# Optimization experiments

Hardware: AMD Instinct MI355X
Metric: run time of the kernel (lower is better)

The kernel has to match this reference:

```python
import jax, jax.numpy as jnp
import numpy as np

MAX_STEP = 4
G_HID = 16      # hidden_graph_num
S_HID = 10      # hidden_graph_size
D = 128         # embed_dim / hidden_dim
N = 100000      # total nodes across batch of session graphs
E = 640000      # total edges
B = 2048        # number of graphs (fixed num_segments)
VOCAB = 100000  # POI vocabulary
NEG_SLOPE = 0.01  # LeakyReLU default


def leaky(x):
    return jnp.where(x >= 0, x, NEG_SLOPE * x)


def setup_inputs() -> dict:
    key = jax.random.key(0)
    ks = jax.random.split(key, 10)
    x_idx = jax.random.randint(ks[0], (N,), 0, VOCAB)
    edge_index = jax.random.randint(ks[1], (2, E), 0, N)
    batch = jnp.sort(jax.random.randint(ks[2], (N,), 0, B))
    poi_emb = jax.random.normal(ks[3], (VOCAB, D), jnp.float32) * 0.02
    fc_w = jax.random.normal(ks[4], (D, D), jnp.float32) / np.sqrt(D)
    fc_b = jnp.zeros((D,), jnp.float32)
    hidden_adj = jax.random.normal(ks[5], (G_HID, S_HID * (S_HID - 1) // 2), jnp.float32)
    hidden_feat = jax.random.normal(ks[6], (G_HID, S_HID, D), jnp.float32)
    mlp_w = jax.random.normal(ks[7], (G_HID * MAX_STEP, D), jnp.float32) / np.sqrt(G_HID * MAX_STEP)
    mlp_b = jnp.zeros((D,), jnp.float32)
    return dict(x_idx=x_idx, edge_index=edge_index, batch=batch,
                poi_emb=poi_emb, fc_w=fc_w, fc_b=fc_b,
                hidden_adj=hidden_adj, hidden_feat=hidden_feat,
                mlp_w=mlp_w, mlp_b=mlp_b)


def reference(x_idx, edge_index, batch, poi_emb, fc_w, fc_b,
              hidden_adj, hidden_feat, mlp_w, mlp_b):
    # Symmetric hidden-graph adjacency from upper-triangular params
    iu, ju = np.triu_indices(S_HID, 1)
    A = jnp.zeros((G_HID, S_HID, S_HID), hidden_adj.dtype).at[:, iu, ju].set(leaky(hidden_adj))
    A = A + jnp.swapaxes(A, 1, 2)

    # Node features: embedding lookup -> Linear -> sigmoid  [N, D]
    x = jax.nn.sigmoid(poi_emb[x_idx] @ fc_w + fc_b)
    z = hidden_feat                                   # [G, S, D]
    zx = jnp.einsum('gsd,nd->gsn', z, x)              # [G, S, N]

    src, dst = edge_index[0], edge_index[1]
    outs = []
    for i in range(MAX_STEP):
        if i == 0:
            # eye @ z == z, so t == zx (faithful to the torch einsum chain)
            t = zx
        else:
            # MessagePassing.propagate with default add aggregation:
            # x_new[v] = sum_{(u->v) in E} x[u]
            x = jax.ops.segment_sum(x[src], dst, num_segments=N)
            z = jnp.einsum('gst,gtd->gsd', A, z)
            t = jnp.einsum('gsd,nd->gsn', z, x)
        t = zx * t                                    # dropout = identity (eval)
        # graph-wise scatter pooling: index_add over node axis -> [B, G, S]
        pooled = jax.ops.segment_sum(jnp.moveaxis(t, 2, 0), batch, num_segments=B)
        outs.append(pooled.sum(axis=2))               # [B, G]

    out = jnp.concatenate(outs, axis=1)               # [B, G*MAX_STEP]
    return leaky(out @ mlp_w + mlp_b)                 # [B, D]
```

## Files before the change

### kernel.cpp

```cpp
#include <hip/hip_runtime.h>
#include <hip/hip_bf16.h>
#include <math.h>

#define G_HID 16
#define S_HID 10
#define D 128
#define MAX_STEP 4
#define NEG 0.01f
#define SCAN_TILE 1024

typedef __attribute__((ext_vector_type(8))) short short8;
typedef __attribute__((ext_vector_type(4))) float f32x4;

__device__ __forceinline__ float leaky_f(float v){ return v >= 0.f ? v : NEG*v; }
__device__ __forceinline__ unsigned short f2bf(float f){
    unsigned int u = __float_as_uint(f);
    u = (u + 0x7FFFu + ((u>>16)&1u)) >> 16;
    return (unsigned short)u;
}
__device__ __forceinline__ float bf_lo(unsigned int v){ return __uint_as_float(v << 16); }
__device__ __forceinline__ float bf_hi(unsigned int v){ return __uint_as_float(v & 0xFFFF0000u); }

__global__ void prep_kernel(const float* __restrict__ hidden_adj,
                            const float* __restrict__ hidden_feat,
                            short* __restrict__ zpack)
{
    int g = blockIdx.x;
    __shared__ float Ag[S_HID][S_HID];
    __shared__ float zb[2][S_HID][D];
    int t = threadIdx.x;
    if (t < S_HID*S_HID) {
        int i = t / S_HID, j = t % S_HID;
        float v = 0.f;
        if (i < j) {
            int idx = 9*i - i*(i-1)/2 + (j - i - 1);
            v = leaky_f(hidden_adj[g*45 + idx]);
        } else if (i > j) {
            int idx = 9*j - j*(j-1)/2 + (i - j - 1);
            v = leaky_f(hidden_adj[g*45 + idx]);
        }
        Ag[i][j] = v;
    }
    for (int idx = t; idx < S_HID*D; idx += 128) {
        int s = idx / D, d = idx % D;
        zb[0][s][d] = hidden_feat[(g*S_HID + s)*D + d];
    }
    __syncthreads();
    int cur = 0;
    for (int step = 0; step < MAX_STEP; ++step) {
        if (step > 0) {
            int nxt = cur ^ 1;
            for (int idx = t; idx < S_HID*D; idx += 128) {
                int s = idx / D, d = idx % D;
                float acc = 0.f;
                #pragma unroll
                for (int u = 0; u < S_HID; ++u) acc += Ag[s][u] * zb[cur][u][d];
                zb[nxt][s][d] = acc;
            }
            cur = nxt;
            __syncthreads();
        }
        for (int idx = t; idx < S_HID*D; idx += 128) {
            int s = idx / D, k = idx % D;
            int row = g*S_HID + s;
            int tt = row >> 4, li = row & 15;
            int kt = k >> 5, q = (k >> 3) & 3, j = k & 7;
            zpack[(((step*10 + tt)*4 + kt)*64 + q*16 + li)*8 + j] = (short)f2bf(zb[cur][s][k]);
        }
        __syncthreads();
    }
}

__global__ void wpack_kernel(const float* __restrict__ fc_w, short* __restrict__ wp){
    int idx = blockIdx.x*256 + threadIdx.x;
    if (idx >= 16384) return;
    int j = idx & 7, lane = (idx >> 3) & 63, ctkt = idx >> 9;
    int ct = ctkt & 7, kt = ctkt >> 3;
    int k   = kt*32 + (lane >> 4)*8 + j;
    int col = ct*16 + (lane & 15);
    wp[idx] = (short)f2bf(fc_w[k*D + col]);
}

__global__ void count_kernel(const int* __restrict__ dst, int* __restrict__ offsets, int E){
    int e = blockIdx.x*blockDim.x + threadIdx.x;
    if (e < E) atomicAdd(&offsets[dst[e]+1], 1);
}

__global__ void scan1_kernel(int* __restrict__ data, int* __restrict__ bsums, int n){
    __shared__ int wsum[4];
    int base = blockIdx.x * SCAN_TILE + threadIdx.x*4;
    int v[4];
    #pragma unroll
    for (int j=0;j<4;++j) v[j] = (base+j < n) ? data[base+j] : 0;
    v[1]+=v[0]; v[2]+=v[1]; v[3]+=v[2];
    int lane = threadIdx.x & 63;
    int w = threadIdx.x >> 6;
    int s = v[3];
    for (int d=1; d<64; d<<=1){
        int o = __shfl_up(s, d);
        if (lane >= d) s += o;
    }
    if (lane == 63) wsum[w] = s;
    int sexc = s - v[3];
    __syncthreads();
    int woff = 0;
    for (int ww=0; ww<w; ++ww) woff += wsum[ww];
    int off = woff + sexc;
    #pragma unroll
    for (int j=0;j<4;++j) { if (base+j < n) data[base+j] = v[j] + off; }
    if (threadIdx.x == 255) bsums[blockIdx.x] = off + v[3];
}

__global__ void scan2_kernel(int* __restrict__ bsums, int nb){
    __shared__ int ws[4];
    __shared__ int carry_s;
    if (threadIdx.x == 0) carry_s = 0;
    __syncthreads();
    for (int start = 0; start < nb; start += 256){
        int i = start + (int)threadIdx.x;
        int v = (i < nb) ? bsums[i] : 0;
        int lane = threadIdx.x & 63, w = threadIdx.x >> 6;
        int s = v;
        for (int d=1; d<64; d<<=1){ int o = __shfl_up(s, d); if (lane >= d) s += o; }
        if (lane == 63) ws[w] = s;
        __syncthreads();
        int woff = 0;
        for (int ww=0; ww<w; ++ww) woff += ws[ww];
        int inc = s + woff + carry_s;
        if (i < nb) bsums[i] = inc - v;
        __syncthreads();
        if (threadIdx.x == 255) carry_s = inc;
        __syncthreads();
    }
}

__global__ void scan3_kernel(int* __restrict__ data, const int* __restrict__ bsums, int n){
    int base = blockIdx.x * SCAN_TILE + threadIdx.x*4;
    int add = bsums[blockIdx.x];
    #pragma unroll
    for (int j=0;j<4;++j){ if (base+j < n) data[base+j] += add; }
}

__global__ void fill_kernel(const int* __restrict__ src, const int* __restrict__ dst,
                            int* __restrict__ cursor, int* __restrict__ csr, int E){
    int e = blockIdx.x*blockDim.x + threadIdx.x;
    if (e < E){
        int d = dst[e];
        int pos = atomicAdd(&cursor[d], 1);
        csr[pos] = src[e];
    }
}


__device__ __forceinline__ void compute_slots(const int* __restrict__ batch, int n0, int N,
                                              int* slots, int* slotb, int* nslots_s, int t){
    if (t < 64) {
        int gn = n0 + t;
        int b = (gn < N) ? batch[gn] : -1;
        int bprev = -1;
        if (t > 0) bprev = (gn-1 < N) ? batch[gn-1] : -1;
        int flag = (t == 0 || b != bprev) ? 1 : 0;
        int s = flag;
        for (int d=1; d<64; d<<=1){ int o = __shfl_up(s, d); if (t >= d) s += o; }
        int slot = s - 1;
        slots[t] = slot;
        if (flag) slotb[slot] = b;
        if (t == 63) *nslots_s = s;
    }
}

template<int STEP0>
__device__ __forceinline__ void step_phase(const short8 bw[4],
                                 const short* __restrict__ zstep,
                                 float* Pf, float (*accs)[G_HID],
                                 const int* slots, const int* slotb, int nslots,
                                 uint2* __restrict__ y0buf, float* __restrict__ pooled,
                                 int stepoff, int t, int bid)
{
    int l = t & 63, w = t >> 6, li = l & 15, q = l >> 4;
    f32x4 accA[10];
    #pragma unroll
    for (int t10 = 0; t10 < 10; ++t10){
        f32x4 acc = (f32x4){0.f,0.f,0.f,0.f};
        #pragma unroll
        for (int kt = 0; kt < 4; ++kt){
            short8 az = *reinterpret_cast<const short8*>(&zstep[((t10*4 + kt)*64 + l)*8]);
            acc = __builtin_amdgcn_mfma_f32_16x16x32_bf16(az, bw[kt], acc, 0, 0, 0);
        }
        accA[t10] = acc;
    }
    size_t ybase = ((size_t)bid*4 + w)*10*64 + l;
    #pragma unroll
    for (int t10 = 0; t10 < 10; ++t10){
        f32x4 acc = accA[t10];
        float p0, p1, p2, p3;
        if (STEP0){
            uint2 st;
            st.x = (unsigned int)f2bf(acc[0]) | ((unsigned int)f2bf(acc[1]) << 16);
            st.y = (unsigned int)f2bf(acc[2]) | ((unsigned int)f2bf(acc[3]) << 16);
            y0buf[ybase + (size_t)t10*64] = st;
            p0 = acc[0]*acc[0]; p1 = acc[1]*acc[1]; p2 = acc[2]*acc[2]; p3 = acc[3]*acc[3];
        } else {
            uint2 v = y0buf[ybase + (size_t)t10*64];
            p0 = acc[0]*bf_lo(v.x); p1 = acc[1]*bf_hi(v.x);
            p2 = acc[2]*bf_lo(v.y); p3 = acc[3]*bf_hi(v.y);
        }
        int rb = (t10*16 + q*4)*66 + w*16 + li;
        Pf[rb]       = p0;
        Pf[rb + 66]  = p1;
        Pf[rb + 132] = p2;
        Pf[rb + 198] = p3;
    }
    __syncthreads();
    #pragma unroll
    for (int i = 0; i < 4; ++i){
        int g = t & 15, nd = (t >> 4) + i*16;
        float c = 0.f;
        #pragma unroll
        for (int s = 0; s < S_HID; ++s) c += Pf[(g*10 + s)*66 + nd];
        atomicAdd(&accs[slots[nd]][g], c);
    }
    __syncthreads();
    for (int idx = t; idx < nslots*G_HID; idx += 256){
        int j = idx >> 4, g = idx & 15;
        int b = slotb[j];
        if (b >= 0) atomicAdd(&pooled[(size_t)b*64 + stepoff + g], accs[j][g]);
    }
}

__global__ __launch_bounds__(256) void embed_step0_kernel(
        const int* __restrict__ x_idx, const float* __restrict__ poi_emb,
        const short* __restrict__ wp, const float* __restrict__ fc_b,
        const short* __restrict__ zstep, const int* __restrict__ batch,
        unsigned short* __restrict__ x0, uint2* __restrict__ y0buf,
        float* __restrict__ pooled, int N)
{
    __shared__ __align__(16) char lbuf[42240];
    __shared__ float accs[64][G_HID];
    __shared__ int slots[64];
    __shared__ int slotb[64];
    __shared__ int nslots_s;
    unsigned short* xs = (unsigned short*)lbuf;
    float* Pf = (float*)lbuf;
    int n0 = blockIdx.x * 64;
    int t = threadIdx.x;

    #pragma unroll
    for (int i = 0; i < 8; ++i) {
        int idx = t + i*256;
        int row = idx >> 5, c4 = (idx & 31)*4;
        int gn = n0 + row;
        float4 v = make_float4(0.f,0.f,0.f,0.f);
        if (gn < N) v = *reinterpret_cast<const float4*>(&poi_emb[(size_t)x_idx[gn]*D + c4]);
        unsigned int p0 = (unsigned int)f2bf(v.x) | ((unsigned int)f2bf(v.y) << 16);
        unsigned int p1 = (unsigned int)f2bf(v.z) | ((unsigned int)f2bf(v.w) << 16);
        *reinterpret_cast<uint2*>(&xs[row*136 + c4]) = make_uint2(p0, p1);
    }
    #pragma unroll
    for (int i = 0; i < 4; ++i) ((float*)accs)[t + i*256] = 0.f;
    compute_slots(batch, n0, N, slots, slotb, &nslots_s, t);
    __syncthreads();

    int l = t & 63, w = t >> 6, li = l & 15, q = l >> 4;
    short8 a[4];
    #pragma unroll
    for (int kt = 0; kt < 4; ++kt)
        a[kt] = *reinterpret_cast<const short8*>(&xs[(w*16 + li)*136 + kt*32 + q*8]);
    f32x4 facc[8];
    #pragma unroll
    for (int ct = 0; ct < 8; ++ct) facc[ct] = (f32x4){0.f,0.f,0.f,0.f};
    #pragma unroll
    for (int kt = 0; kt < 4; ++kt){
        #pragma unroll
        for (int ct = 0; ct < 8; ++ct){
            short8 b = reinterpret_cast<const short8*>(wp)[(kt*8 + ct)*64 + l];
            facc[ct] = __builtin_amdgcn_mfma_f32_16x16x32_bf16(a[kt], b, facc[ct], 0, 0, 0);
        }
    }
    #pragma unroll
    for (int ct = 0; ct < 8; ++ct){
        float bias = fc_b[ct*16 + li];
        #pragma unroll
        for (int r = 0; r < 4; ++r){
            int row = w*16 + q*4 + r;
            float s = (n0 + row < N) ? 1.f/(1.f + __expf(-(facc[ct][r] + bias))) : 0.f;
            xs[row*136 + ct*16 + li] = f2bf(s);
        }
    }
    __syncthreads();
    {
        int row = t >> 2, ch = t & 3, gn = n0 + row;
        if (gn < N){
            #pragma unroll
            for (int i2 = 0; i2 < 4; ++i2){
                uint4 v = *reinterpret_cast<const uint4*>(&xs[row*136 + ch*32 + i2*8]);
                *reinterpret_cast<uint4*>(&x0[(size_t)gn*D + ch*32 + i2*8]) = v;
            }
        }
    }
    short8 bw[4];
    #pragma unroll
    for (int kt = 0; kt < 4; ++kt)
        bw[kt] = *reinterpret_cast<const short8*>(&xs[(w*16 + li)*136 + kt*32 + q*8]);
    __syncthreads();

    step_phase<1>(bw, zstep, Pf, accs, slots, slotb, nslots_s,
                  y0buf, pooled, 0, t, blockIdx.x);
}

template<int WRITE_X>
__global__ __launch_bounds__(256) void prop_step_kernel(
        const unsigned short* __restrict__ xin, unsigned short* __restrict__ xout,
        const int* __restrict__ offsets, const int* __restrict__ csr,
        const short* __restrict__ zstep, const int* __restrict__ batch,
        uint2* __restrict__ y0buf, float* __restrict__ pooled,
        int N, int stepoff)
{
    __shared__ __align__(16) char lbuf[42240];
    __shared__ float accs[64][G_HID];
    __shared__ int slots[64];
    __shared__ int slotb[64];
    __shared__ int nslots_s;
    unsigned short* xs = (unsigned short*)lbuf;
    float* Pf = (float*)lbuf;
    int n0 = blockIdx.x * 64;
    int t = threadIdx.x;
    int l = t & 63, w = t >> 6, li = l & 15, q = l >> 4;
    int c = l & 15;

    #pragma unroll
    for (int i = 0; i < 4; ++i) ((float*)accs)[t + i*256] = 0.f;
    compute_slots(batch, n0, N, slots, slotb, &nslots_s, t);

    const uint4* xi4 = (const uint4*)xin;
    for (int nn = 0; nn < 4; ++nn){
        int lrow = w*16 + nn*4 + q;
        int node = n0 + lrow;
        float a[8];
        #pragma unroll
        for (int j=0;j<8;++j) a[j] = 0.f;
        if (node < N){
            int beg = offsets[node], end = offsets[node+1];
            for (int base = beg; base < end; base += 16){
                int cnt = min(16, end - base);
                int myu = (base + c < end) ? csr[base + c] : 0;
                for (int ei = 0; ei < cnt; ++ei){
                    int u = __shfl(myu, (q<<4) + ei);
                    uint4 va = xi4[(size_t)u*16 + c];
                    a[0] += bf_lo(va.x); a[1] += bf_hi(va.x);
                    a[2] += bf_lo(va.y); a[3] += bf_hi(va.y);
                    a[4] += bf_lo(va.z); a[5] += bf_hi(va.z);
                    a[6] += bf_lo(va.w); a[7] += bf_hi(va.w);
                }
            }
        }
        uint4 o;
        o.x = (unsigned int)f2bf(a[0]) | ((unsigned int)f2bf(a[1]) << 16);
        o.y = (unsigned int)f2bf(a[2]) | ((unsigned int)f2bf(a[3]) << 16);
        o.z = (unsigned int)f2bf(a[4]) | ((unsigned int)f2bf(a[5]) << 16);
        o.w = (unsigned int)f2bf(a[6]) | ((unsigned int)f2bf(a[7]) << 16);
        *reinterpret_cast<uint4*>(&xs[lrow*136 + c*8]) = o;
        if (WRITE_X && node < N) ((uint4*)xout)[(size_t)node*16 + c] = o;
    }
    __syncthreads();

    short8 bw[4];
    #pragma unroll
    for (int kt = 0; kt < 4; ++kt)
        bw[kt] = *reinterpret_cast<const short8*>(&xs[(w*16 + li)*136 + kt*32 + q*8]);
    __syncthreads();

    step_phase<0>(bw, zstep, Pf, accs, slots, slotb, nslots_s,
                  y0buf, pooled, stepoff, t, blockIdx.x);
}

__global__ void out_kernel(const float* __restrict__ pooled, const float* __restrict__ mlp_w,
                           const float* __restrict__ mlp_b, float* __restrict__ out, int B){
    __shared__ float row[64];
    int b = blockIdx.x;
    int t = threadIdx.x;
    if (t < 64) row[t] = pooled[(size_t)b*64 + t];
    __syncthreads();
    float acc = mlp_b[t];
    for (int j=0;j<64;++j) acc += row[j]*mlp_w[j*D + t];
    out[(size_t)b*D + t] = leaky_f(acc);
}

extern "C" void kernel_launch(void* const* d_in, const int* in_sizes, int n_in,
                              void* d_out, int out_size, void* d_ws, size_t ws_size,
                              hipStream_t stream)
{
    const int*   x_idx = (const int*)d_in[0];
    const int*   edge  = (const int*)d_in[1];
    const int*   batch = (const int*)d_in[2];
    const float* poi   = (const float*)d_in[3];
    const float* fc_w  = (const float*)d_in[4];
    const float* fc_b  = (const float*)d_in[5];
    const float* adj   = (const float*)d_in[6];
    const float* feat  = (const float*)d_in[7];
    const float* mlp_w = (const float*)d_in[8];
    const float* mlp_b = (const float*)d_in[9];
    float* out = (float*)d_out;

    int N = in_sizes[0];
    int E = in_sizes[1] / 2;
    int B = out_size / D;
    int sblk = (N + 63) / 64;
    size_t NP = (size_t)sblk * 64;

    char* p = (char*)d_ws;
    auto alloc = [&](size_t bytes)->char* {
        char* r = p;
        p += (bytes + 255) & ~(size_t)255;
        return r;
    };
    unsigned short* x0 = (unsigned short*)alloc(NP*D*2);
    unsigned short* xa = (unsigned short*)alloc(NP*D*2);
    unsigned short* xb = (unsigned short*)alloc(NP*D*2);
    uint2* y0buf       = (uint2*)alloc(NP*160*2);
    float* pooled      = (float*)alloc((size_t)B*64*4);
    short* zpack       = (short*)alloc((size_t)MAX_STEP*20480*2);
    short* wp          = (short*)alloc((size_t)16384*2);
    int*   offsets     = (int*)alloc((size_t)(N+1)*4);
    int*   cursor      = (int*)alloc((size_t)N*4);
    int*   csr         = (int*)alloc((size_t)E*4);
    int*   bsums       = (int*)alloc(4096);

    const int* srcp = edge;
    const int* dstp = edge + E;

    hipMemsetAsync(offsets, 0, (size_t)(N+1)*4, stream);
    hipMemsetAsync(pooled, 0, (size_t)B*64*4, stream);

    prep_kernel<<<G_HID, 128, 0, stream>>>(adj, feat, zpack);
    wpack_kernel<<<64, 256, 0, stream>>>(fc_w, wp);

    count_kernel<<<(E+255)/256, 256, 0, stream>>>(dstp, offsets, E);
    int scan_n = N + 1;
    int nblk = (scan_n + SCAN_TILE - 1) / SCAN_TILE;
    scan1_kernel<<<nblk, 256, 0, stream>>>(offsets, bsums, scan_n);
    scan2_kernel<<<1, 256, 0, stream>>>(bsums, nblk);
    scan3_kernel<<<nblk, 256, 0, stream>>>(offsets, bsums, scan_n);
    hipMemcpyAsync(cursor, offsets, (size_t)N*4, hipMemcpyDeviceToDevice, stream);
    fill_kernel<<<(E+255)/256, 256, 0, stream>>>(srcp, dstp, cursor, csr, E);

    embed_step0_kernel<<<sblk, 256, 0, stream>>>(x_idx, poi, wp, fc_b, zpack, batch,
                                                 x0, y0buf, pooled, N);

    const unsigned short* xin = x0;
    unsigned short* bufs[2] = {xa, xb};
    for (int i = 1; i < MAX_STEP; ++i){
        unsigned short* xout = bufs[(i-1) & 1];
        if (i < MAX_STEP-1)
            prop_step_kernel<1><<<sblk, 256, 0, stream>>>(xin, xout, offsets, csr,
                                  zpack + (size_t)i*20480, batch, y0buf, pooled, N, i*G_HID);
        else
            prop_step_kernel<0><<<sblk, 256, 0, stream>>>(xin, xout, offsets, csr,
                                  zpack + (size_t)i*20480, batch, y0buf, pooled, N, i*G_HID);
        xin = xout;
    }
    out_kernel<<<B, D, 0, stream>>>(pooled, mlp_w, mlp_b, out, B);
}
```

Measured before the change: 382.0 us.

## Propagate projected 160-dim features instead of 128-dim node embeddings

Uses linearity: (z_i x_i) for step i equals A^i z applied to propagated projections of x, so the kernel propagates W = z0·x (160 values per node) through the graph instead of raw 128-dim x, and applies precomputed powers A, A², A³ per group. This removes the per-step MFMA projection and the separate x buffers. Propagation is now one wave per node with 40-lane uint2 gathers. CSR fill also uses ranks from the count atomics instead of a second atomic pass. The trade-offs are a 25% larger gathered row per edge, idle lanes (40 of 64), and per-node global atomics into pooled.

```diff
diff --git a/kernel.cpp b/kernel.cpp
--- a/kernel.cpp
+++ b/kernel.cpp
@@ -8,6 +8,7 @@
 #define MAX_STEP 4
 #define NEG 0.01f
 #define SCAN_TILE 1024
+#define YT_PITCH 168
 
 typedef __attribute__((ext_vector_type(8))) short short8;
 typedef __attribute__((ext_vector_type(4))) float f32x4;
@@ -20,14 +21,17 @@
 }
 __device__ __forceinline__ float bf_lo(unsigned int v){ return __uint_as_float(v << 16); }
 __device__ __forceinline__ float bf_hi(unsigned int v){ return __uint_as_float(v & 0xFFFF0000u); }
+__device__ __forceinline__ float bfu(unsigned short u){ return __uint_as_float(((unsigned int)u) << 16); }
 
 __global__ void prep_kernel(const float* __restrict__ hidden_adj,
                             const float* __restrict__ hidden_feat,
-                            short* __restrict__ zpack)
+                            short* __restrict__ zpack,
+                            float* __restrict__ Ai)
 {
     int g = blockIdx.x;
     __shared__ float Ag[S_HID][S_HID];
-    __shared__ float zb[2][S_HID][D];
+    __shared__ float A2[S_HID][S_HID];
+    __shared__ float A3[S_HID][S_HID];
     int t = threadIdx.x;
     if (t < S_HID*S_HID) {
         int i = t / S_HID, j = t % S_HID;
@@ -41,33 +45,31 @@
         }
         Ag[i][j] = v;
     }
+    __syncthreads();
+    if (t < 100){
+        int s = t/10, u = t%10;
+        float c = 0.f;
+        #pragma unroll
+        for (int w = 0; w < 10; ++w) c += Ag[s][w]*Ag[w][u];
+        A2[s][u] = c;
+    }
+    __syncthreads();
+    if (t < 100){
+        int s = t/10, u = t%10;
+        float c = 0.f;
+        #pragma unroll
+        for (int w = 0; w < 10; ++w) c += A2[s][w]*Ag[w][u];
+        A3[s][u] = c;
+        Ai[0*1600 + g*100 + t] = Ag[s][u];
+        Ai[1*1600 + g*100 + t] = A2[s][u];
+        Ai[2*1600 + g*100 + t] = A3[s][u];
+    }
     for (int idx = t; idx < S_HID*D; idx += 128) {
-        int s = idx / D, d = idx % D;
-        zb[0][s][d] = hidden_feat[(g*S_HID + s)*D + d];
-    }
-    __syncthreads();
-    int cur = 0;
-    for (int step = 0; step < MAX_STEP; ++step) {
-        if (step > 0) {
-            int nxt = cur ^ 1;
-            for (int idx = t; idx < S_HID*D; idx += 128) {
-                int s = idx / D, d = idx % D;
-                float acc = 0.f;
-                #pragma unroll
-                for (int u = 0; u < S_HID; ++u) acc += Ag[s][u] * zb[cur][u][d];
-                zb[nxt][s][d] = acc;
-            }
-            cur = nxt;
-            __syncthreads();
-        }
-        for (int idx = t; idx < S_HID*D; idx += 128) {
-            int s = idx / D, k = idx % D;
-            int row = g*S_HID + s;
-            int tt = row >> 4, li = row & 15;
-            int kt = k >> 5, q = (k >> 3) & 3, j = k & 7;
-            zpack[(((step*10 + tt)*4 + kt)*64 + q*16 + li)*8 + j] = (short)f2bf(zb[cur][s][k]);
-        }
-        __syncthreads();
+        int s = idx / D, k = idx % D;
+        int row = g*S_HID + s;
+        int tt = row >> 4, li = row & 15;
+        int kt = k >> 5, q = (k >> 3) & 3, j = k & 7;
+        zpack[((tt*4 + kt)*64 + q*16 + li)*8 + j] = (short)f2bf(hidden_feat[(g*S_HID + s)*D + k]);
     }
 }
 
@@ -81,9 +83,10 @@
     wp[idx] = (short)f2bf(fc_w[k*D + col]);
 }
 
-__global__ void count_kernel(const int* __restrict__ dst, int* __restrict__ offsets, int E){
+__global__ void count_kernel(const int* __restrict__ dst, int* __restrict__ offsets,
+                             int* __restrict__ rnk, int E){
     int e = blockIdx.x*blockDim.x + threadIdx.x;
-    if (e < E) atomicAdd(&offsets[dst[e]+1], 1);
+    if (e < E) rnk[e] = atomicAdd(&offsets[dst[e]+1], 1);
 }
 
 __global__ void scan1_kernel(int* __restrict__ data, int* __restrict__ bsums, int n){
@@ -142,15 +145,11 @@
 }
 
 __global__ void fill_kernel(const int* __restrict__ src, const int* __restrict__ dst,
-                            int* __restrict__ cursor, int* __restrict__ csr, int E){
+                            const int* __restrict__ rnk, const int* __restrict__ offsets,
+                            int* __restrict__ csr, int E){
     int e = blockIdx.x*blockDim.x + threadIdx.x;
-    if (e < E){
-        int d = dst[e];
-        int pos = atomicAdd(&cursor[d], 1);
-        csr[pos] = src[e];
-    }
-}
-
+    if (e < E) csr[offsets[dst[e]] + rnk[e]] = src[e];
+}
 
 __device__ __forceinline__ void compute_slots(const int* __restrict__ batch, int n0, int N,
                                               int* slots, int* slotb, int* nslots_s, int t){
@@ -169,79 +168,20 @@
     }
 }
 
-template<int STEP0>
-__device__ __forceinline__ void step_phase(const short8 bw[4],
-                                 const short* __restrict__ zstep,
-                                 float* Pf, float (*accs)[G_HID],
-                                 const int* slots, const int* slotb, int nslots,
-                                 uint2* __restrict__ y0buf, float* __restrict__ pooled,
-                                 int stepoff, int t, int bid)
-{
-    int l = t & 63, w = t >> 6, li = l & 15, q = l >> 4;
-    f32x4 accA[10];
-    #pragma unroll
-    for (int t10 = 0; t10 < 10; ++t10){
-        f32x4 acc = (f32x4){0.f,0.f,0.f,0.f};
-        #pragma unroll
-        for (int kt = 0; kt < 4; ++kt){
-            short8 az = *reinterpret_cast<const short8*>(&zstep[((t10*4 + kt)*64 + l)*8]);
-            acc = __builtin_amdgcn_mfma_f32_16x16x32_bf16(az, bw[kt], acc, 0, 0, 0);
-        }
-        accA[t10] = acc;
-    }
-    size_t ybase = ((size_t)bid*4 + w)*10*64 + l;
-    #pragma unroll
-    for (int t10 = 0; t10 < 10; ++t10){
-        f32x4 acc = accA[t10];
-        float p0, p1, p2, p3;
-        if (STEP0){
-            uint2 st;
-            st.x = (unsigned int)f2bf(acc[0]) | ((unsigned int)f2bf(acc[1]) << 16);
-            st.y = (unsigned int)f2bf(acc[2]) | ((unsigned int)f2bf(acc[3]) << 16);
-            y0buf[ybase + (size_t)t10*64] = st;
-            p0 = acc[0]*acc[0]; p1 = acc[1]*acc[1]; p2 = acc[2]*acc[2]; p3 = acc[3]*acc[3];
-        } else {
-            uint2 v = y0buf[ybase + (size_t)t10*64];
-            p0 = acc[0]*bf_lo(v.x); p1 = acc[1]*bf_hi(v.x);
-            p2 = acc[2]*bf_lo(v.y); p3 = acc[3]*bf_hi(v.y);
-        }
-        int rb = (t10*16 + q*4)*66 + w*16 + li;
-        Pf[rb]       = p0;
-        Pf[rb + 66]  = p1;
-        Pf[rb + 132] = p2;
-        Pf[rb + 198] = p3;
-    }
-    __syncthreads();
-    #pragma unroll
-    for (int i = 0; i < 4; ++i){
-        int g = t & 15, nd = (t >> 4) + i*16;
-        float c = 0.f;
-        #pragma unroll
-        for (int s = 0; s < S_HID; ++s) c += Pf[(g*10 + s)*66 + nd];
-        atomicAdd(&accs[slots[nd]][g], c);
-    }
-    __syncthreads();
-    for (int idx = t; idx < nslots*G_HID; idx += 256){
-        int j = idx >> 4, g = idx & 15;
-        int b = slotb[j];
-        if (b >= 0) atomicAdd(&pooled[(size_t)b*64 + stepoff + g], accs[j][g]);
-    }
-}
-
 __global__ __launch_bounds__(256) void embed_step0_kernel(
         const int* __restrict__ x_idx, const float* __restrict__ poi_emb,
         const short* __restrict__ wp, const float* __restrict__ fc_b,
-        const short* __restrict__ zstep, const int* __restrict__ batch,
-        unsigned short* __restrict__ x0, uint2* __restrict__ y0buf,
+        const short* __restrict__ zpack, const int* __restrict__ batch,
+        unsigned short* __restrict__ W0,
         float* __restrict__ pooled, int N)
 {
-    __shared__ __align__(16) char lbuf[42240];
+    __shared__ __align__(16) char lbuf[64*YT_PITCH*2];
     __shared__ float accs[64][G_HID];
     __shared__ int slots[64];
     __shared__ int slotb[64];
     __shared__ int nslots_s;
-    unsigned short* xs = (unsigned short*)lbuf;
-    float* Pf = (float*)lbuf;
+    unsigned short* xs  = (unsigned short*)lbuf;
+    unsigned short* ytr = (unsigned short*)lbuf;
     int n0 = blockIdx.x * 64;
     int t = threadIdx.x;
 
@@ -256,8 +196,7 @@
         unsigned int p1 = (unsigned int)f2bf(v.z) | ((unsigned int)f2bf(v.w) << 16);
         *reinterpret_cast<uint2*>(&xs[row*136 + c4]) = make_uint2(p0, p1);
     }
-    #pragma unroll
-    for (int i = 0; i < 4; ++i) ((float*)accs)[t + i*256] = 0.f;
+    for (int idx = t; idx < 64*G_HID; idx += 256) ((float*)accs)[idx] = 0.f;
     compute_slots(batch, n0, N, slots, slotb, &nslots_s, t);
     __syncthreads();
 
@@ -288,90 +227,144 @@
         }
     }
     __syncthreads();
-    {
-        int row = t >> 2, ch = t & 3, gn = n0 + row;
-        if (gn < N){
-            #pragma unroll
-            for (int i2 = 0; i2 < 4; ++i2){
-                uint4 v = *reinterpret_cast<const uint4*>(&xs[row*136 + ch*32 + i2*8]);
-                *reinterpret_cast<uint4*>(&x0[(size_t)gn*D + ch*32 + i2*8]) = v;
-            }
-        }
-    }
     short8 bw[4];
     #pragma unroll
     for (int kt = 0; kt < 4; ++kt)
         bw[kt] = *reinterpret_cast<const short8*>(&xs[(w*16 + li)*136 + kt*32 + q*8]);
     __syncthreads();
 
-    step_phase<1>(bw, zstep, Pf, accs, slots, slotb, nslots_s,
-                  y0buf, pooled, 0, t, blockIdx.x);
-}
-
-template<int WRITE_X>
-__global__ __launch_bounds__(256) void prop_step_kernel(
-        const unsigned short* __restrict__ xin, unsigned short* __restrict__ xout,
+    #pragma unroll
+    for (int t10 = 0; t10 < 10; ++t10){
+        f32x4 acc = (f32x4){0.f,0.f,0.f,0.f};
+        #pragma unroll
+        for (int kt = 0; kt < 4; ++kt){
+            short8 az = *reinterpret_cast<const short8*>(&zpack[((t10*4 + kt)*64 + l)*8]);
+            acc = __builtin_amdgcn_mfma_f32_16x16x32_bf16(az, bw[kt], acc, 0, 0, 0);
+        }
+        uint2 pk;
+        pk.x = (unsigned int)f2bf(acc[0]) | ((unsigned int)f2bf(acc[1]) << 16);
+        pk.y = (unsigned int)f2bf(acc[2]) | ((unsigned int)f2bf(acc[3]) << 16);
+        *reinterpret_cast<uint2*>(&ytr[(w*16 + li)*YT_PITCH + t10*16 + q*4]) = pk;
+    }
+    __syncthreads();
+
+    {
+        int nd = t >> 2, part = t & 3, gn = n0 + nd;
+        if (gn < N){
+            const uint2* srcl = reinterpret_cast<const uint2*>(&ytr[nd*YT_PITCH + part*40]);
+            uint2* dstg = reinterpret_cast<uint2*>(&W0[(size_t)gn*160 + part*40]);
+            #pragma unroll
+            for (int k2 = 0; k2 < 10; ++k2) dstg[k2] = srcl[k2];
+        }
+    }
+    #pragma unroll
+    for (int i = 0; i < 4; ++i){
+        int nd2 = t & 63;
+        int g = (t >> 6) + i*4;
+        if (n0 + nd2 < N){
+            float c = 0.f;
+            #pragma unroll
+            for (int s = 0; s < S_HID; ++s){
+                float y = bfu(ytr[nd2*YT_PITCH + g*10 + s]);
+                c += y*y;
+            }
+            atomicAdd(&accs[slots[nd2]][g], c);
+        }
+    }
+    __syncthreads();
+    int ns = nslots_s;
+    for (int idx = t; idx < ns*G_HID; idx += 256){
+        int j = idx >> 4, g = idx & 15;
+        int b = slotb[j];
+        if (b >= 0) atomicAdd(&pooled[(size_t)b*64 + g], accs[j][g]);
+    }
+}
+
+__global__ __launch_bounds__(256) void propw_kernel(
+        const uint2* __restrict__ Win, uint2* __restrict__ Wout,
+        const uint2* __restrict__ Y0,
         const int* __restrict__ offsets, const int* __restrict__ csr,
-        const short* __restrict__ zstep, const int* __restrict__ batch,
-        uint2* __restrict__ y0buf, float* __restrict__ pooled,
+        const float* __restrict__ Ai_g,
+        const int* __restrict__ batch, float* __restrict__ pooled,
         int N, int stepoff)
 {
-    __shared__ __align__(16) char lbuf[42240];
-    __shared__ float accs[64][G_HID];
-    __shared__ int slots[64];
-    __shared__ int slotb[64];
-    __shared__ int nslots_s;
-    unsigned short* xs = (unsigned short*)lbuf;
-    float* Pf = (float*)lbuf;
-    int n0 = blockIdx.x * 64;
+    __shared__ float Aw[1600];
+    __shared__ float ylds[4][160];
+    __shared__ float gacc[4][16];
     int t = threadIdx.x;
-    int l = t & 63, w = t >> 6, li = l & 15, q = l >> 4;
-    int c = l & 15;
-
-    #pragma unroll
-    for (int i = 0; i < 4; ++i) ((float*)accs)[t + i*256] = 0.f;
-    compute_slots(batch, n0, N, slots, slotb, &nslots_s, t);
-
-    const uint4* xi4 = (const uint4*)xin;
-    for (int nn = 0; nn < 4; ++nn){
-        int lrow = w*16 + nn*4 + q;
-        int node = n0 + lrow;
-        float a[8];
-        #pragma unroll
-        for (int j=0;j<8;++j) a[j] = 0.f;
-        if (node < N){
-            int beg = offsets[node], end = offsets[node+1];
-            for (int base = beg; base < end; base += 16){
-                int cnt = min(16, end - base);
-                int myu = (base + c < end) ? csr[base + c] : 0;
-                for (int ei = 0; ei < cnt; ++ei){
-                    int u = __shfl(myu, (q<<4) + ei);
-                    uint4 va = xi4[(size_t)u*16 + c];
-                    a[0] += bf_lo(va.x); a[1] += bf_hi(va.x);
-                    a[2] += bf_lo(va.y); a[3] += bf_hi(va.y);
-                    a[4] += bf_lo(va.z); a[5] += bf_hi(va.z);
-                    a[6] += bf_lo(va.w); a[7] += bf_hi(va.w);
-                }
+    for (int idx = t; idx < 1600; idx += 256) Aw[idx] = Ai_g[idx];
+    __syncthreads();
+
+    int wv = t >> 6, l = t & 63;
+    int v = blockIdx.x*4 + wv;
+    if (v >= N) return;
+
+    int beg = offsets[v], end = offsets[v+1];
+    float a0=0.f, a1=0.f, a2=0.f, a3=0.f;
+    for (int base = beg; base < end; base += 64){
+        int cnt = min(64, end - base);
+        int myu = (base + l < end) ? csr[base + l] : 0;
+        int ei = 0;
+        for (; ei + 4 <= cnt; ei += 4){
+            int u0 = __shfl(myu, ei), u1 = __shfl(myu, ei+1);
+            int u2 = __shfl(myu, ei+2), u3 = __shfl(myu, ei+3);
+            uint2 w0 = make_uint2(0,0), w1 = w0, w2 = w0, w3 = w0;
+            if (l < 40){
+                w0 = Win[(size_t)u0*40 + l];
+                w1 = Win[(size_t)u1*40 + l];
+                w2 = Win[(size_t)u2*40 + l];
+                w3 = Win[(size_t)u3*40 + l];
             }
-        }
-        uint4 o;
-        o.x = (unsigned int)f2bf(a[0]) | ((unsigned int)f2bf(a[1]) << 16);
-        o.y = (unsigned int)f2bf(a[2]) | ((unsigned int)f2bf(a[3]) << 16);
-        o.z = (unsigned int)f2bf(a[4]) | ((unsigned int)f2bf(a[5]) << 16);
-        o.w = (unsigned int)f2bf(a[6]) | ((unsigned int)f2bf(a[7]) << 16);
-        *reinterpret_cast<uint4*>(&xs[lrow*136 + c*8]) = o;
-        if (WRITE_X && node < N) ((uint4*)xout)[(size_t)node*16 + c] = o;
-    }
-    __syncthreads();
-
-    short8 bw[4];
-    #pragma unroll
-    for (int kt = 0; kt < 4; ++kt)
-        bw[kt] = *reinterpret_cast<const short8*>(&xs[(w*16 + li)*136 + kt*32 + q*8]);
-    __syncthreads();
-
-    step_phase<0>(bw, zstep, Pf, accs, slots, slotb, nslots_s,
-                  y0buf, pooled, stepoff, t, blockIdx.x);
+            a0 += bf_lo(w0.x) + bf_lo(w1.x) + bf_lo(w2.x) + bf_lo(w3.x);
+            a1 += bf_hi(w0.x) + bf_hi(w1.x) + bf_hi(w2.x) + bf_hi(w3.x);
+            a2 += bf_lo(w0.y) + bf_lo(w1.y) + bf_lo(w2.y) + bf_lo(w3.y);
+            a3 += bf_hi(w0.y) + bf_hi(w1.y) + bf_hi(w2.y) + bf_hi(w3.y);
+        }
+        for (; ei < cnt; ++ei){
+            int u = __shfl(myu, ei);
+            uint2 wv2 = make_uint2(0,0);
+            if (l < 40) wv2 = Win[(size_t)u*40 + l];
+            a0 += bf_lo(wv2.x); a1 += bf_hi(wv2.x);
+            a2 += bf_lo(wv2.y); a3 += bf_hi(wv2.y);
+        }
+    }
+    if (l < 40){
+        uint2 o;
+        o.x = (unsigned int)f2bf(a0) | ((unsigned int)f2bf(a1) << 16);
+        o.y = (unsigned int)f2bf(a2) | ((unsigned int)f2bf(a3) << 16);
+        Wout[(size_t)v*40 + l] = o;
+        uint2 y = Y0[(size_t)v*40 + l];
+        float4 yf;
+        yf.x = bf_lo(y.x); yf.y = bf_hi(y.x); yf.z = bf_lo(y.y); yf.w = bf_hi(y.y);
+        *reinterpret_cast<float4*>(&ylds[wv][l*4]) = yf;
+    }
+    if (l < 16) gacc[wv][l] = 0.f;
+    __threadfence_block();
+
+    if (l < 40){
+        float aj[4] = {a0, a1, a2, a3};
+        int idx0 = 4*l;
+        int ga = idx0/10, gb = (idx0+3)/10;
+        float c0 = 0.f, c1 = 0.f;
+        #pragma unroll
+        for (int j = 0; j < 4; ++j){
+            int idx = idx0 + j;
+            int g = idx/10, s = idx - g*10;
+            float u0v = 0.f;
+            #pragma unroll
+            for (int tt = 0; tt < 10; ++tt)
+                u0v += Aw[g*100 + s*10 + tt] * ylds[wv][g*10 + tt];
+            float p = u0v * aj[j];
+            if (g == ga) c0 += p; else c1 += p;
+        }
+        atomicAdd(&gacc[wv][ga], c0);
+        if (gb != ga) atomicAdd(&gacc[wv][gb], c1);
+    }
+    __threadfence_block();
+    if (l < 16){
+        int b = batch[v];
+        atomicAdd(&pooled[(size_t)b*64 + stepoff + l], gacc[wv][l]);
+    }
 }
 
 __global__ void out_kernel(const float* __restrict__ pooled, const float* __restrict__ mlp_w,
@@ -414,15 +407,15 @@
         p += (bytes + 255) & ~(size_t)255;
         return r;
     };
-    unsigned short* x0 = (unsigned short*)alloc(NP*D*2);
-    unsigned short* xa = (unsigned short*)alloc(NP*D*2);
-    unsigned short* xb = (unsigned short*)alloc(NP*D*2);
-    uint2* y0buf       = (uint2*)alloc(NP*160*2);
+    unsigned short* Y0 = (unsigned short*)alloc(NP*160*2);
+    unsigned short* Wa = (unsigned short*)alloc(NP*160*2);
+    unsigned short* Wb = (unsigned short*)alloc(NP*160*2);
     float* pooled      = (float*)alloc((size_t)B*64*4);
-    short* zpack       = (short*)alloc((size_t)MAX_STEP*20480*2);
+    short* zpack       = (short*)alloc((size_t)20480*2);
     short* wp          = (short*)alloc((size_t)16384*2);
+    float* Ai          = (float*)alloc((size_t)3*1600*4);
     int*   offsets     = (int*)alloc((size_t)(N+1)*4);
-    int*   cursor      = (int*)alloc((size_t)N*4);
+    int*   rnk         = (int*)alloc((size_t)E*4);
     int*   csr         = (int*)alloc((size_t)E*4);
     int*   bsums       = (int*)alloc(4096);
 
@@ -432,32 +425,28 @@
     hipMemsetAsync(offsets, 0, (size_t)(N+1)*4, stream);
     hipMemsetAsync(pooled, 0, (size_t)B*64*4, stream);
 
-    prep_kernel<<<G_HID, 128, 0, stream>>>(adj, feat, zpack);
+    prep_kernel<<<G_HID, 128, 0, stream>>>(adj, feat, zpack, Ai);
     wpack_kernel<<<64, 256, 0, stream>>>(fc_w, wp);
 
-    count_kernel<<<(E+255)/256, 256, 0, stream>>>(dstp, offsets, E);
+    count_kernel<<<(E+255)/256, 256, 0, stream>>>(dstp, offsets, rnk, E);
     int scan_n = N + 1;
     int nblk = (scan_n + SCAN_TILE - 1) / SCAN_TILE;
     scan1_kernel<<<nblk, 256, 0, stream>>>(offsets, bsums, scan_n);
     scan2_kernel<<<1, 256, 0, stream>>>(bsums, nblk);
     scan3_kernel<<<nblk, 256, 0, stream>>>(offsets, bsums, scan_n);
-    hipMemcpyAsync(cursor, offsets, (size_t)N*4, hipMemcpyDeviceToDevice, stream);
-    fill_kernel<<<(E+255)/256, 256, 0, stream>>>(srcp, dstp, cursor, csr, E);
+    fill_kernel<<<(E+255)/256, 256, 0, stream>>>(srcp, dstp, rnk, offsets, csr, E);
 
     embed_step0_kernel<<<sblk, 256, 0, stream>>>(x_idx, poi, wp, fc_b, zpack, batch,
-                                                 x0, y0buf, pooled, N);
-
-    const unsigned short* xin = x0;
-    unsigned short* bufs[2] = {xa, xb};
+                                                 Y0, pooled, N);
+
+    const unsigned short* win = Y0;
+    unsigned short* bufs[2] = {Wa, Wb};
     for (int i = 1; i < MAX_STEP; ++i){
-        unsigned short* xout = bufs[(i-1) & 1];
-        if (i < MAX_STEP-1)
-            prop_step_kernel<1><<<sblk, 256, 0, stream>>>(xin, xout, offsets, csr,
-                                  zpack + (size_t)i*20480, batch, y0buf, pooled, N, i*G_HID);
-        else
-            prop_step_kernel<0><<<sblk, 256, 0, stream>>>(xin, xout, offsets, csr,
-                                  zpack + (size_t)i*20480, batch, y0buf, pooled, N, i*G_HID);
-        xin = xout;
+        unsigned short* wout = bufs[(i-1) & 1];
+        propw_kernel<<<(N+3)/4, 256, 0, stream>>>(
+            (const uint2*)win, (uint2*)wout, (const uint2*)Y0,
+            offsets, csr, Ai + (size_t)(i-1)*1600, batch, pooled, N, i*G_HID);
+        win = wout;
     }
     out_kernel<<<B, D, 0, stream>>>(pooled, mlp_w, mlp_b, out, B);
 }
```

After: 399.0 us. +4.4%, slower.
